# Kernel tuning notes

Hardware: AMD Instinct MI355X
Metric: run time of the kernel (lower is better)

Reference implementation:

```python
import jax, jax.numpy as jnp
import numpy as np

V = 100000   # vocab_size
E = 256      # embedding_dim
H = 256      # hidden_dim // 2 (per direction)
T = 32       # tagset_size
S = 4096     # seq_len
START, STOP = 30, 31
NEG = -10000.0


def setup_inputs() -> dict:
    key = jax.random.key(0)
    ks = jax.random.split(key, 13)
    sentence = jax.random.randint(ks[0], (S,), 0, V)
    h0 = jax.random.normal(ks[1], (2, H), dtype=jnp.float32)
    c0 = jax.random.normal(ks[2], (2, H), dtype=jnp.float32)
    embedding = jax.random.normal(ks[3], (V, E), dtype=jnp.float32) * 0.1
    # LSTM params, PyTorch layout: gates [i, f, g, o], combined bias = b_ih + b_hh
    w_ih_f = jax.random.normal(ks[4], (4 * H, E), dtype=jnp.float32) * 0.05
    w_hh_f = jax.random.normal(ks[5], (4 * H, H), dtype=jnp.float32) * 0.05
    b_f = jax.random.normal(ks[6], (4 * H,), dtype=jnp.float32) * 0.05
    w_ih_b = jax.random.normal(ks[7], (4 * H, E), dtype=jnp.float32) * 0.05
    w_hh_b = jax.random.normal(ks[8], (4 * H, H), dtype=jnp.float32) * 0.05
    b_b = jax.random.normal(ks[9], (4 * H,), dtype=jnp.float32) * 0.05
    lin_w = jax.random.normal(ks[10], (T, 2 * H), dtype=jnp.float32) * 0.05
    lin_b = jax.random.normal(ks[11], (T,), dtype=jnp.float32) * 0.05
    transitions = jax.random.normal(ks[12], (T, T), dtype=jnp.float32)
    transitions = transitions.at[START, :].set(NEG).at[:, STOP].set(NEG)
    return {"sentence": sentence, "h0": h0, "c0": c0, "embedding": embedding,
            "w_ih_f": w_ih_f, "w_hh_f": w_hh_f, "b_f": b_f,
            "w_ih_b": w_ih_b, "w_hh_b": w_hh_b, "b_b": b_b,
            "lin_w": lin_w, "lin_b": lin_b, "transitions": transitions}


def _lstm_dir(emb, h0, c0, w_ih, w_hh, b):
    # Precompute input contribution for all timesteps: [S, 4H]
    xg = emb @ w_ih.T + b

    def step(carry, xt):
        h, c = carry
        g = xt + h @ w_hh.T
        i, f, gg, o = jnp.split(g, 4)
        i = jax.nn.sigmoid(i); f = jax.nn.sigmoid(f)
        gg = jnp.tanh(gg); o = jax.nn.sigmoid(o)
        c = f * c + i * gg
        h = o * jnp.tanh(c)
        return (h, c), h

    _, hs = jax.lax.scan(step, (h0, c0), xg)
    return hs  # [S, H]


def reference(sentence, h0, c0, embedding, w_ih_f, w_hh_f, b_f,
              w_ih_b, w_hh_b, b_b, lin_w, lin_b, transitions):
    emb = embedding[sentence]                                    # [S, E]
    hs_f = _lstm_dir(emb, h0[0], c0[0], w_ih_f, w_hh_f, b_f)     # [S, H]
    hs_b = _lstm_dir(emb[::-1], h0[1], c0[1], w_ih_b, w_hh_b, b_b)[::-1]
    feats = jnp.concatenate([hs_f, hs_b], axis=-1) @ lin_w.T + lin_b  # [S, T]

    # Viterbi: forward_var over tags, vectorized over next/prev tags
    init = jnp.full((T,), NEG, dtype=feats.dtype).at[START].set(0.0)

    def vit_step(fv, feat):
        scores = fv[None, :] + transitions    # [next_tag, prev_tag]
        bp = jnp.argmax(scores, axis=1)       # best prev for each next tag
        fv_new = jnp.max(scores, axis=1) + feat
        return fv_new, bp

    fv, bps = jax.lax.scan(vit_step, init, feats)  # bps: [S, T]
    final = fv + transitions[STOP]
    last = jnp.argmax(final)
    score = final[last]

    # Backtrack (reverse scan); outputs[t] = best tag at timestep t
    def back_step(idx, bp):
        return bp[idx], idx

    _, path = jax.lax.scan(back_step, last, bps, reverse=True)
    return score, path
```

## Files before the change

### kernel.cpp

```cpp
#include <hip/hip_runtime.h>
#include <cstdint>
#include <cstddef>

#define S 4096
#define E 256
#define H 256
#define T 32
#define START_TAG 30
#define STOP_TAG 31
#define NEGV (-10000.0f)

typedef _Float16 half_t;
typedef _Float16 h2 __attribute__((ext_vector_type(2)));
typedef _Float16 f16x8 __attribute__((ext_vector_type(8)));
typedef float f32x4 __attribute__((ext_vector_type(4)));

__device__ __forceinline__ unsigned short f2h16(float f) {
    half_t h = (half_t)f;
    unsigned short u; __builtin_memcpy(&u, &h, 2); return u;
}
__device__ __forceinline__ float h16tof(unsigned short u) {
    half_t h; __builtin_memcpy(&h, &u, 2); return (float)h;
}

__device__ __forceinline__ float sigmoidf_(float x) {
    return 1.0f / (1.0f + __expf(-x));
}
__device__ __forceinline__ float tanhf_(float x) {
    return 1.0f - 2.0f / (__expf(2.0f * x) + 1.0f);
}

__device__ __forceinline__ f16x8 cvt8(float4 a, float4 b) {
    f16x8 v;
    v[0] = (_Float16)a.x; v[1] = (_Float16)a.y; v[2] = (_Float16)a.z; v[3] = (_Float16)a.w;
    v[4] = (_Float16)b.x; v[5] = (_Float16)b.y; v[6] = (_Float16)b.z; v[7] = (_Float16)b.w;
    return v;
}

#define SBLK 16
__global__ __launch_bounds__(256) void xg_kernel(
    const int* __restrict__ sent, const float* __restrict__ emb,
    const float* __restrict__ w_ih_f, const float* __restrict__ b_f,
    const float* __restrict__ w_ih_b, const float* __restrict__ b_b,
    unsigned short* __restrict__ xg16s)
{
    const int dir = blockIdx.y;
    const int t0 = blockIdx.x * SBLK;
    const float* w_ih = dir ? w_ih_b : w_ih_f;
    const float* bias = dir ? b_b : b_f;

    __shared__ float embs[SBLK][E];
    for (int p = threadIdx.x; p < SBLK * (E / 4); p += 256) {
        int r = p >> 6, kq = p & 63;
        int t = t0 + r;
        int tt = dir ? (S - 1 - t) : t;
        int tok = sent[tt];
        float4 v = *(const float4*)(emb + (size_t)tok * E + 4 * kq);
        *(float4*)&embs[r][4 * kq] = v;
    }
    __syncthreads();

    for (int jj = 0; jj < 4; ++jj) {
        int j = jj * 256 + threadIdx.x;
        const float* wrow = w_ih + (size_t)j * E;
        float bv = bias[j];
        float acc[SBLK];
        #pragma unroll
        for (int t = 0; t < SBLK; ++t) acc[t] = bv;

        for (int kc = 0; kc < E / 16; ++kc) {
            float w[16];
            float4 a0 = *(const float4*)(wrow + kc * 16);
            float4 a1 = *(const float4*)(wrow + kc * 16 + 4);
            float4 a2 = *(const float4*)(wrow + kc * 16 + 8);
            float4 a3 = *(const float4*)(wrow + kc * 16 + 12);
            float wv[16] = { a0.x, a0.y, a0.z, a0.w, a1.x, a1.y, a1.z, a1.w,
                             a2.x, a2.y, a2.z, a2.w, a3.x, a3.y, a3.z, a3.w };
            #pragma unroll
            for (int q = 0; q < 16; ++q) w[q] = wv[q];
            #pragma unroll
            for (int t = 0; t < SBLK; ++t) {
                const float* er = &embs[t][kc * 16];
                float s = 0.f;
                #pragma unroll
                for (int q = 0; q < 16; ++q) s += w[q] * er[q];
                acc[t] += s;
            }
        }
        const int u = threadIdx.x;
        #pragma unroll
        for (int t = 0; t < SBLK; ++t) {
            size_t base = (((size_t)dir * S + (size_t)(t0 + t)) * 256 + u) * 4 + jj;
            xg16s[base] = f2h16(acc[t]);
        }
    }
}

#define WLDS_BYTES (8 * 8 * 2 * 64 * 16)
#define LSTM_LDS_BYTES (WLDS_BYTES + 2 * 256 * 2)

__global__ __launch_bounds__(512, 2) void lstm_kernel(
    const float* __restrict__ h0, const float* __restrict__ c0,
    const float* __restrict__ w_hh_f, const float* __restrict__ w_hh_b,
    const unsigned long long* __restrict__ xgq, float* __restrict__ hs)
{
    extern __shared__ char smem[];

    const int dir  = blockIdx.x;
    const int tid  = threadIdx.x;
    const int lane = tid & 63;
    const int w    = tid >> 6;
    const int n    = lane & 15;
    const int kg   = lane >> 4;
    const float* w_hh = dir ? w_hh_b : w_hh_f;

    char* fragp = smem + ((size_t)w * 16 * 1024) + (size_t)lane * 16;

    f16x8 wR[8][6];
    #pragma unroll
    for (int c = 0; c < 8; ++c) {
        const int row = (c & 3) * 256 + w * 32 + 2 * n + (c >> 2);
        const float* pr = w_hh + (size_t)row * H + kg * 8;
        #pragma unroll
        for (int kt = 0; kt < 6; ++kt) {
            float4 a = *(const float4*)(pr + kt * 32);
            float4 b = *(const float4*)(pr + kt * 32 + 4);
            wR[c][kt] = cvt8(a, b);
        }
        #pragma unroll
        for (int j = 0; j < 2; ++j) {
            float4 a = *(const float4*)(pr + (6 + j) * 32);
            float4 b = *(const float4*)(pr + (6 + j) * 32 + 4);
            f16x8 v = cvt8(a, b);
            *(f16x8*)(fragp + (c * 2 + j) * 1024) = v;
        }
    }

    const int  u_a    = w * 32 + 2 * n;
    const bool hiU    = (kg >= 2);
    const int  u_own  = u_a + (hiU ? 1 : 0);
    const bool writer = (kg == 0) || (kg == 2);
    float cst = c0[dir * H + u_own];

    _Float16* hb0 = (_Float16*)(smem + WLDS_BYTES);
    if (tid < 256) hb0[tid] = (_Float16)h0[dir * H + tid];

    const unsigned long long* xgl = xgq + (size_t)dir * S * 256 + u_own;
    unsigned long long xgw = xgl[0];

    __syncthreads();

    for (int t = 0; t < S; ++t) {
        const char* hbp = smem + WLDS_BYTES + ((t & 1) << 9) + kg * 16;

        const int tn = (t + 1 < S) ? (t + 1) : t;
        unsigned long long xgn = xgl[(size_t)tn * 256];

        f32x4 acc[8];
        const f32x4 zc = { 0.f, 0.f, 0.f, 0.f };

        {
            f16x8 hA6 = *(const f16x8*)(hbp + 6 * 64);
            f16x8 hA7 = *(const f16x8*)(hbp + 7 * 64);
            #pragma unroll
            for (int c = 0; c < 8; ++c) {
                f16x8 w6 = *(const f16x8*)(fragp + (c * 2 + 0) * 1024);
                f16x8 w7 = *(const f16x8*)(fragp + (c * 2 + 1) * 1024);
                acc[c] = __builtin_amdgcn_mfma_f32_16x16x32_f16(hA6, w6, zc, 0, 0, 0);
                acc[c] = __builtin_amdgcn_mfma_f32_16x16x32_f16(hA7, w7, acc[c], 0, 0, 0);
            }
        }
        #pragma unroll
        for (int kt = 0; kt < 6; ++kt) {
            f16x8 hA = *(const f16x8*)(hbp + kt * 64);
            #pragma unroll
            for (int c = 0; c < 8; ++c)
                acc[c] = __builtin_amdgcn_mfma_f32_16x16x32_f16(hA, wR[c][kt], acc[c], 0, 0, 0);
        }

        unsigned int lo = (unsigned int)xgw;
        unsigned int hi = (unsigned int)(xgw >> 32);

        float gi = (hiU ? acc[4][0] : acc[0][0]) + h16tof((unsigned short)(lo & 0xffffu));
        float gf = (hiU ? acc[5][0] : acc[1][0]) + h16tof((unsigned short)(lo >> 16));
        float gg = (hiU ? acc[6][0] : acc[2][0]) + h16tof((unsigned short)(hi & 0xffffu));
        float go = (hiU ? acc[7][0] : acc[3][0]) + h16tof((unsigned short)(hi >> 16));

        float iv = sigmoidf_(gi);
        float fv = sigmoidf_(gf);
        float gv = tanhf_(gg);
        float ov = sigmoidf_(go);
        cst = fv * cst + iv * gv;
        float hv = ov * tanhf_(cst);

        if (writer) {
            *(_Float16*)(smem + WLDS_BYTES + (((t + 1) & 1) << 9) + u_own * 2) = (_Float16)hv;
            int row = dir ? (S - 1 - t) : t;
            hs[(size_t)row * 512 + dir * 256 + u_own] = hv;
        }
        xgw = xgn;
        __syncthreads();
    }
}

__global__ __launch_bounds__(256) void feats_kernel(
    const float* __restrict__ hs, const float* __restrict__ lin_w,
    const float* __restrict__ lin_b, float* __restrict__ feats)
{
    const int t0 = blockIdx.x * 8;
    __shared__ float rows[8][512];
    for (int p = threadIdx.x; p < 8 * 128; p += 256) {
        int r = p >> 7, sg = p & 127;
        float4 v = *(const float4*)(hs + (size_t)(t0 + r) * 512 + sg * 4);
        *(float4*)&rows[r][sg * 4] = v;
    }
    __syncthreads();

    const int tl = threadIdx.x >> 5, tag = threadIdx.x & 31;
    const float* lw = lin_w + (size_t)tag * 512;
    float acc = lin_b[tag];
    for (int kc = 0; kc < 32; ++kc) {
        float4 a0 = *(const float4*)(lw + kc * 16);
        float4 a1 = *(const float4*)(lw + kc * 16 + 4);
        float4 a2 = *(const float4*)(lw + kc * 16 + 8);
        float4 a3 = *(const float4*)(lw + kc * 16 + 12);
        const float* er = &rows[tl][kc * 16];
        acc += a0.x * er[0] + a0.y * er[1] + a0.z * er[2] + a0.w * er[3];
        acc += a1.x * er[4] + a1.y * er[5] + a1.z * er[6] + a1.w * er[7];
        acc += a2.x * er[8] + a2.y * er[9] + a2.z * er[10] + a2.w * er[11];
        acc += a3.x * er[12] + a3.y * er[13] + a3.z * er[14] + a3.w * er[15];
    }
    feats[(size_t)(t0 + tl) * T + tag] = acc;
}

#define VCS 64
#define VNC (S / VCS)
__global__ __launch_bounds__(256) void vit_chunk_kernel(
    const float* __restrict__ feats, const float* __restrict__ trans,
    float* __restrict__ gM)
{
    const int c = blockIdx.x;
    const int tid = threadIdx.x;
    const int n = tid >> 3, p0 = (tid & 7) * 4;
    __shared__ float Mb[2][32][36];

    float tr[32];
    #pragma unroll
    for (int k = 0; k < 32; ++k) tr[k] = trans[n * 32 + k];

    float f0 = feats[(size_t)(c * VCS) * 32 + n];
    float4 cur = { tr[p0] + f0, tr[p0 + 1] + f0, tr[p0 + 2] + f0, tr[p0 + 3] + f0 };
    *(float4*)&Mb[0][n][p0] = cur;
    __syncthreads();

    int rb = 0;
    for (int s = 1; s < VCS; ++s) {
        float fn = feats[(size_t)(c * VCS + s) * 32 + n];
        float4 acc = { -3.0e38f, -3.0e38f, -3.0e38f, -3.0e38f };
        #pragma unroll 8
        for (int k = 0; k < 32; ++k) {
            float4 mo = *(const float4*)&Mb[rb][k][p0];
            float tk = tr[k];
            acc.x = fmaxf(acc.x, tk + mo.x);
            acc.y = fmaxf(acc.y, tk + mo.y);
            acc.z = fmaxf(acc.z, tk + mo.z);
            acc.w = fmaxf(acc.w, tk + mo.w);
        }
        acc.x += fn; acc.y += fn; acc.z += fn; acc.w += fn;
        cur = acc;
        *(float4*)&Mb[rb ^ 1][n][p0] = acc;
        rb ^= 1;
        __syncthreads();
    }
    *(float4*)(gM + (size_t)c * 1024 + n * 32 + p0) = cur;
}

__global__ __launch_bounds__(1024) void vit_combine_kernel(
    const float* __restrict__ feats, const float* __restrict__ trans,
    const float* __restrict__ gM, unsigned char* __restrict__ gbp,
    float* __restrict__ out)
{
    __shared__ float MS[1024];
    __shared__ __align__(16) float bfv[VNC + 1][32];
    __shared__ __align__(16) float fvc[VNC][32];
    __shared__ unsigned char Mmap[VNC][32];
    __shared__ int ent[VNC];
    __shared__ int lastsh;

    const int tid = threadIdx.x;

    if (tid < 32) bfv[0][tid] = (tid == START_TAG) ? 0.f : NEGV;
    __syncthreads();
    for (int c = 0; c < VNC; ++c) {
        MS[tid] = gM[(size_t)c * 1024 + tid];
        __syncthreads();
        if (tid < 32) {
            float m = -3.0e38f;
            #pragma unroll 8
            for (int k = 0; k < 32; ++k)
                m = fmaxf(m, MS[tid * 32 + k] + bfv[c][k]);
            bfv[c + 1][tid] = m;
        }
        __syncthreads();
    }
    if (tid == 0) {
        float bm = -3.0e38f; int bl = 0;
        for (int j = 0; j < 32; ++j) {
            float s2 = bfv[VNC][j] + trans[STOP_TAG * 32 + j];
            if (s2 > bm) { bm = s2; bl = j; }
        }
        out[0] = bm;
        lastsh = bl;
    }
    __syncthreads();

    for (int pass = 0; pass < 2; ++pass) {
        const int c = (tid >> 5) + pass * 32;
        const int nt = tid & 31;
        float tr[32];
        #pragma unroll
        for (int k = 0; k < 32; ++k) tr[k] = trans[nt * 32 + k];

        fvc[c][nt] = bfv[c][nt];
        __builtin_amdgcn_wave_barrier();
        asm volatile("" ::: "memory");

        for (int s = 0; s < VCS; ++s) {
            const int t = c * VCS + s;
            float4 v0 = *(const float4*)&fvc[c][0];
            float4 v1 = *(const float4*)&fvc[c][4];
            float4 v2 = *(const float4*)&fvc[c][8];
            float4 v3 = *(const float4*)&fvc[c][12];
            float4 v4 = *(const float4*)&fvc[c][16];
            float4 v5 = *(const float4*)&fvc[c][20];
            float4 v6 = *(const float4*)&fvc[c][24];
            float4 v7 = *(const float4*)&fvc[c][28];
            float fvv[32] = { v0.x, v0.y, v0.z, v0.w, v1.x, v1.y, v1.z, v1.w,
                              v2.x, v2.y, v2.z, v2.w, v3.x, v3.y, v3.z, v3.w,
                              v4.x, v4.y, v4.z, v4.w, v5.x, v5.y, v5.z, v5.w,
                              v6.x, v6.y, v6.z, v6.w, v7.x, v7.y, v7.z, v7.w };
            float m = -3.0e38f; int bi = 0;
            #pragma unroll
            for (int k = 0; k < 32; ++k) {
                float s2 = fvv[k] + tr[k];
                if (s2 > m) { m = s2; bi = k; }
            }
            m += feats[(size_t)t * 32 + nt];
            gbp[(size_t)t * 32 + nt] = (unsigned char)bi;
            __builtin_amdgcn_wave_barrier();
            asm volatile("" ::: "memory");
            fvc[c][nt] = m;
            __builtin_amdgcn_wave_barrier();
            asm volatile("" ::: "memory");
        }
        __syncthreads();
    }

    {
        #pragma unroll
        for (int kk = 0; kk < 2; ++kk) {
            int it = tid + kk * 1024;
            int cc = it >> 5, st = it & 31;
            int cur = st;
            for (int s = VCS - 1; s >= 0; --s)
                cur = gbp[(size_t)(cc * VCS + s) * 32 + cur];
            Mmap[cc][st] = (unsigned char)cur;
        }
    }
    __syncthreads();

    if (tid == 0) {
        int cur = lastsh;
        ent[VNC - 1] = cur;
        for (int cchunk = VNC - 1; cchunk > 0; --cchunk) {
            cur = Mmap[cchunk][cur];
            ent[cchunk - 1] = cur;
        }
    }
    __syncthreads();

    if (tid < VNC) {
        int cur = ent[tid];
        for (int i = VCS - 1; i >= 0; --i) {
            int t = tid * VCS + i;
            out[1 + t] = (float)cur;
            cur = gbp[(size_t)t * 32 + cur];
        }
    }
}

extern "C" void kernel_launch(void* const* d_in, const int* in_sizes, int n_in,
                              void* d_out, int out_size, void* d_ws, size_t ws_size,
                              hipStream_t stream)
{
    const int* sent      = (const int*)d_in[0];
    const float* h0      = (const float*)d_in[1];
    const float* c0      = (const float*)d_in[2];
    const float* emb     = (const float*)d_in[3];
    const float* w_ih_f  = (const float*)d_in[4];
    const float* w_hh_f  = (const float*)d_in[5];
    const float* b_f     = (const float*)d_in[6];
    const float* w_ih_b  = (const float*)d_in[7];
    const float* w_hh_b  = (const float*)d_in[8];
    const float* b_b     = (const float*)d_in[9];
    const float* lin_w   = (const float*)d_in[10];
    const float* lin_b   = (const float*)d_in[11];
    const float* trans   = (const float*)d_in[12];
    float* out = (float*)d_out;

    unsigned long long* xgq = (unsigned long long*)d_ws;
    float* hs    = (float*)(xgq + (size_t)2 * S * 256);
    float* feats = hs + (size_t)S * 512;
    float* gM    = feats + (size_t)S * T;
    unsigned char* gbp = (unsigned char*)(gM + (size_t)VNC * 1024);

    hipFuncSetAttribute((const void*)lstm_kernel,
                        hipFuncAttributeMaxDynamicSharedMemorySize, LSTM_LDS_BYTES);

    xg_kernel<<<dim3(S / SBLK, 2), 256, 0, stream>>>(sent, emb, w_ih_f, b_f, w_ih_b, b_b,
                                                     (unsigned short*)xgq);
    lstm_kernel<<<2, 512, LSTM_LDS_BYTES, stream>>>(h0, c0, w_hh_f, w_hh_b, xgq, hs);
    feats_kernel<<<S / 8, 256, 0, stream>>>(hs, lin_w, lin_b, feats);
    vit_chunk_kernel<<<VNC, 256, 0, stream>>>(feats, trans, gM);
    vit_combine_kernel<<<1, 1024, 0, stream>>>(feats, trans, gM, gbp, out);
}
```

Baseline: 6.312 ms.

## Stream one k-tile of recurrent weights from global/L2 instead of LDS

Adds a prep kernel that packs the k-tile 6 fragments of w_hh into fp16 MFMA layout in global memory. The LSTM kernel now keeps only k-tile 7 in LDS and reloads the k-tile 6 fragments from global (cached in L2) every timestep, interleaving the loads with the MFMA chain. The aim is to cut per-step LDS traffic on the serial recurrence by moving part of the weight reads to the vector memory path. The cost is global-load latency inside the critical loop, plus one extra kernel launch.

```diff
diff --git a/kernel.cpp b/kernel.cpp
--- a/kernel.cpp
+++ b/kernel.cpp
@@ -11,7 +11,6 @@
 #define NEGV (-10000.0f)
 
 typedef _Float16 half_t;
-typedef _Float16 h2 __attribute__((ext_vector_type(2)));
 typedef _Float16 f16x8 __attribute__((ext_vector_type(8)));
 typedef float f32x4 __attribute__((ext_vector_type(4)));
 
@@ -35,6 +34,30 @@
     v[0] = (_Float16)a.x; v[1] = (_Float16)a.y; v[2] = (_Float16)a.z; v[3] = (_Float16)a.w;
     v[4] = (_Float16)b.x; v[5] = (_Float16)b.y; v[6] = (_Float16)b.z; v[7] = (_Float16)b.w;
     return v;
+}
+
+__global__ __launch_bounds__(512) void wprep_kernel(
+    const float* __restrict__ w_hh_f, const float* __restrict__ w_hh_b,
+    uint4* __restrict__ frag6)
+{
+    const int dir  = blockIdx.x;
+    const int tid  = threadIdx.x;
+    const int lane = tid & 63;
+    const int w    = tid >> 6;
+    const int n    = lane & 15;
+    const int kg   = lane >> 4;
+    const float* w_hh = dir ? w_hh_b : w_hh_f;
+
+    #pragma unroll
+    for (int c = 0; c < 8; ++c) {
+        const int row = (c & 3) * 256 + w * 32 + 2 * n + (c >> 2);
+        const float* pr = w_hh + (size_t)row * H + 6 * 32 + kg * 8;
+        float4 a = *(const float4*)(pr);
+        float4 b = *(const float4*)(pr + 4);
+        f16x8 v = cvt8(a, b);
+        uint4 u; __builtin_memcpy(&u, &v, 16);
+        frag6[((size_t)(dir * 8 + w) * 8 + c) * 64 + lane] = u;
+    }
 }
 
 #define SBLK 16
@@ -96,13 +119,14 @@
     }
 }
 
-#define WLDS_BYTES (8 * 8 * 2 * 64 * 16)
+#define WLDS_BYTES (8 * 8 * 64 * 16)
 #define LSTM_LDS_BYTES (WLDS_BYTES + 2 * 256 * 2)
 
 __global__ __launch_bounds__(512, 2) void lstm_kernel(
     const float* __restrict__ h0, const float* __restrict__ c0,
     const float* __restrict__ w_hh_f, const float* __restrict__ w_hh_b,
-    const unsigned long long* __restrict__ xgq, float* __restrict__ hs)
+    const unsigned long long* __restrict__ xgq, const uint4* __restrict__ frag6,
+    float* __restrict__ hs)
 {
     extern __shared__ char smem[];
 
@@ -114,7 +138,7 @@
     const int kg   = lane >> 4;
     const float* w_hh = dir ? w_hh_b : w_hh_f;
 
-    char* fragp = smem + ((size_t)w * 16 * 1024) + (size_t)lane * 16;
+    char* fragp = smem + ((size_t)w * 8192) + (size_t)lane * 16;
 
     f16x8 wR[8][6];
     #pragma unroll
@@ -127,12 +151,11 @@
             float4 b = *(const float4*)(pr + kt * 32 + 4);
             wR[c][kt] = cvt8(a, b);
         }
-        #pragma unroll
-        for (int j = 0; j < 2; ++j) {
-            float4 a = *(const float4*)(pr + (6 + j) * 32);
-            float4 b = *(const float4*)(pr + (6 + j) * 32 + 4);
+        {
+            float4 a = *(const float4*)(pr + 7 * 32);
+            float4 b = *(const float4*)(pr + 7 * 32 + 4);
             f16x8 v = cvt8(a, b);
-            *(f16x8*)(fragp + (c * 2 + j) * 1024) = v;
+            *(f16x8*)(fragp + c * 1024) = v;
         }
     }
 
@@ -148,11 +171,20 @@
     const unsigned long long* xgl = xgq + (size_t)dir * S * 256 + u_own;
     unsigned long long xgw = xgl[0];
 
+    const uint4* fgp = frag6 + (size_t)(dir * 8 + w) * 8 * 64 + lane;
+
     __syncthreads();
 
     for (int t = 0; t < S; ++t) {
         const char* hbp = smem + WLDS_BYTES + ((t & 1) << 9) + kg * 16;
 
+        const uint4* fg0 = fgp;
+        asm volatile("" : "+v"(fg0));
+        uint4 g0 = fg0[0 * 64];
+        uint4 g1 = fg0[1 * 64];
+        uint4 g2 = fg0[2 * 64];
+        uint4 g3 = fg0[3 * 64];
+
         const int tn = (t + 1 < S) ? (t + 1) : t;
         unsigned long long xgn = xgl[(size_t)tn * 256];
 
@@ -160,18 +192,52 @@
         const f32x4 zc = { 0.f, 0.f, 0.f, 0.f };
 
         {
-            f16x8 hA6 = *(const f16x8*)(hbp + 6 * 64);
             f16x8 hA7 = *(const f16x8*)(hbp + 7 * 64);
             #pragma unroll
             for (int c = 0; c < 8; ++c) {
-                f16x8 w6 = *(const f16x8*)(fragp + (c * 2 + 0) * 1024);
-                f16x8 w7 = *(const f16x8*)(fragp + (c * 2 + 1) * 1024);
-                acc[c] = __builtin_amdgcn_mfma_f32_16x16x32_f16(hA6, w6, zc, 0, 0, 0);
-                acc[c] = __builtin_amdgcn_mfma_f32_16x16x32_f16(hA7, w7, acc[c], 0, 0, 0);
+                f16x8 wx = *(const f16x8*)(fragp + c * 1024);
+                acc[c] = __builtin_amdgcn_mfma_f32_16x16x32_f16(hA7, wx, zc, 0, 0, 0);
             }
         }
-        #pragma unroll
-        for (int kt = 0; kt < 6; ++kt) {
+
+        f16x8 hA6 = *(const f16x8*)(hbp + 6 * 64);
+        {
+            f16x8 w0, w1, w2, w3;
+            __builtin_memcpy(&w0, &g0, 16); __builtin_memcpy(&w1, &g1, 16);
+            __builtin_memcpy(&w2, &g2, 16); __builtin_memcpy(&w3, &g3, 16);
+            acc[0] = __builtin_amdgcn_mfma_f32_16x16x32_f16(hA6, w0, acc[0], 0, 0, 0);
+            acc[1] = __builtin_amdgcn_mfma_f32_16x16x32_f16(hA6, w1, acc[1], 0, 0, 0);
+            acc[2] = __builtin_amdgcn_mfma_f32_16x16x32_f16(hA6, w2, acc[2], 0, 0, 0);
+            acc[3] = __builtin_amdgcn_mfma_f32_16x16x32_f16(hA6, w3, acc[3], 0, 0, 0);
+        }
+
+        const uint4* fg1 = fgp + 4 * 64;
+        asm volatile("" : "+v"(fg1));
+        g0 = fg1[0 * 64];
+        g1 = fg1[1 * 64];
+        g2 = fg1[2 * 64];
+        g3 = fg1[3 * 64];
+
+        #pragma unroll
+        for (int kt = 0; kt < 3; ++kt) {
+            f16x8 hA = *(const f16x8*)(hbp + kt * 64);
+            #pragma unroll
+            for (int c = 0; c < 8; ++c)
+                acc[c] = __builtin_amdgcn_mfma_f32_16x16x32_f16(hA, wR[c][kt], acc[c], 0, 0, 0);
+        }
+
+        {
+            f16x8 w4, w5, w6, w7;
+            __builtin_memcpy(&w4, &g0, 16); __builtin_memcpy(&w5, &g1, 16);
+            __builtin_memcpy(&w6, &g2, 16); __builtin_memcpy(&w7, &g3, 16);
+            acc[4] = __builtin_amdgcn_mfma_f32_16x16x32_f16(hA6, w4, acc[4], 0, 0, 0);
+            acc[5] = __builtin_amdgcn_mfma_f32_16x16x32_f16(hA6, w5, acc[5], 0, 0, 0);
+            acc[6] = __builtin_amdgcn_mfma_f32_16x16x32_f16(hA6, w6, acc[6], 0, 0, 0);
+            acc[7] = __builtin_amdgcn_mfma_f32_16x16x32_f16(hA6, w7, acc[7], 0, 0, 0);
+        }
+
+        #pragma unroll
+        for (int kt = 3; kt < 6; ++kt) {
             f16x8 hA = *(const f16x8*)(hbp + kt * 64);
             #pragma unroll
             for (int c = 0; c < 8; ++c)
@@ -413,13 +479,15 @@
     float* feats = hs + (size_t)S * 512;
     float* gM    = feats + (size_t)S * T;
     unsigned char* gbp = (unsigned char*)(gM + (size_t)VNC * 1024);
+    uint4* frag6 = (uint4*)(gbp + (size_t)S * 32);
 
     hipFuncSetAttribute((const void*)lstm_kernel,
                         hipFuncAttributeMaxDynamicSharedMemorySize, LSTM_LDS_BYTES);
 
+    wprep_kernel<<<2, 512, 0, stream>>>(w_hh_f, w_hh_b, frag6);
     xg_kernel<<<dim3(S / SBLK, 2), 256, 0, stream>>>(sent, emb, w_ih_f, b_f, w_ih_b, b_b,
                                                      (unsigned short*)xgq);
-    lstm_kernel<<<2, 512, LSTM_LDS_BYTES, stream>>>(h0, c0, w_hh_f, w_hh_b, xgq, hs);
+    lstm_kernel<<<2, 512, LSTM_LDS_BYTES, stream>>>(h0, c0, w_hh_f, w_hh_b, xgq, frag6, hs);
     feats_kernel<<<S / 8, 256, 0, stream>>>(hs, lin_w, lin_b, feats);
     vit_chunk_kernel<<<VNC, 256, 0, stream>>>(feats, trans, gM);
     vit_combine_kernel<<<1, 1024, 0, stream>>>(feats, trans, gM, gbp, out);
```

Result: slower. 7.622 ms (+20.8%).

## Split recurrent matvec K-range between MFMA and VALU dot2 paths

Applied to the files above, without the earlier changes.

The recurrent h@W_hh product previously ran entirely on MFMA over 8 K-tiles (6 held in registers, 2 read from LDS). Now MFMA covers only 6 K-tiles (4 in registers, 2 in LDS). The last 64 hidden inputs are computed per lane with packed fp16 dot2 instructions on weights held in registers, and the two halves are combined with a cross-lane shuffle. The aim is to shorten the serial MFMA chain on each timestep by running part of the reduction on the vector ALU in parallel. The cost is extra VALU work, more LDS reads and register pressure, and the writer lanes change from kg 0/2 to kg 0/1.

```diff
diff --git a/kernel.cpp b/kernel.cpp
--- a/kernel.cpp
+++ b/kernel.cpp
@@ -15,6 +15,12 @@
 typedef _Float16 f16x8 __attribute__((ext_vector_type(8)));
 typedef float f32x4 __attribute__((ext_vector_type(4)));
 
+__device__ __forceinline__ h2 f2h2(float a, float b) {
+    h2 r; r[0] = (half_t)a; r[1] = (half_t)b; return r;
+}
+__device__ __forceinline__ h2 u2h2(unsigned int u) {
+    h2 r; __builtin_memcpy(&r, &u, 4); return r;
+}
 __device__ __forceinline__ unsigned short f2h16(float f) {
     half_t h = (half_t)f;
     unsigned short u; __builtin_memcpy(&u, &h, 2); return u;
@@ -22,6 +28,16 @@
 __device__ __forceinline__ float h16tof(unsigned short u) {
     half_t h; __builtin_memcpy(&h, &u, 2); return (float)h;
 }
+
+#if __has_builtin(__builtin_amdgcn_fdot2)
+__device__ __forceinline__ float dot2(h2 a, h2 b, float c) {
+    return __builtin_amdgcn_fdot2(a, b, c, false);
+}
+#else
+__device__ __forceinline__ float dot2(h2 a, h2 b, float c) {
+    return c + (float)a[0] * (float)b[0] + (float)a[1] * (float)b[1];
+}
+#endif
 
 __device__ __forceinline__ float sigmoidf_(float x) {
     return 1.0f / (1.0f + __expf(-x));
@@ -116,31 +132,47 @@
 
     char* fragp = smem + ((size_t)w * 16 * 1024) + (size_t)lane * 16;
 
-    f16x8 wR[8][6];
+    f16x8 wR[8][4];
     #pragma unroll
     for (int c = 0; c < 8; ++c) {
         const int row = (c & 3) * 256 + w * 32 + 2 * n + (c >> 2);
         const float* pr = w_hh + (size_t)row * H + kg * 8;
         #pragma unroll
-        for (int kt = 0; kt < 6; ++kt) {
+        for (int kt = 0; kt < 4; ++kt) {
             float4 a = *(const float4*)(pr + kt * 32);
             float4 b = *(const float4*)(pr + kt * 32 + 4);
             wR[c][kt] = cvt8(a, b);
         }
         #pragma unroll
         for (int j = 0; j < 2; ++j) {
-            float4 a = *(const float4*)(pr + (6 + j) * 32);
-            float4 b = *(const float4*)(pr + (6 + j) * 32 + 4);
+            float4 a = *(const float4*)(pr + (4 + j) * 32);
+            float4 b = *(const float4*)(pr + (4 + j) * 32 + 4);
             f16x8 v = cvt8(a, b);
             *(f16x8*)(fragp + (c * 2 + j) * 1024) = v;
         }
     }
 
-    const int  u_a    = w * 32 + 2 * n;
-    const bool hiU    = (kg >= 2);
-    const int  u_own  = u_a + (hiU ? 1 : 0);
-    const bool writer = (kg == 0) || (kg == 2);
+    const int  par    = kg & 1;
+    const int  u_own  = w * 32 + 2 * n + par;
+    const bool writer = (kg < 2);
+    const int  ktvoff = 384 + ((kg >> 1) << 6);
     float cst = c0[dir * H + u_own];
+
+    h2 wV0[16], wV1[16], wV2[16], wV3[16];
+    {
+        const int ktv = 6 + (kg >> 1);
+        #pragma unroll
+        for (int g = 0; g < 4; ++g) {
+            const float* pr = w_hh + (size_t)(g * 256 + u_own) * H + ktv * 32;
+            h2* dst = (g == 0) ? wV0 : (g == 1) ? wV1 : (g == 2) ? wV2 : wV3;
+            #pragma unroll
+            for (int q = 0; q < 8; ++q) {
+                float4 a = *(const float4*)(pr + 4 * q);
+                dst[2 * q]     = f2h2(a.x, a.y);
+                dst[2 * q + 1] = f2h2(a.z, a.w);
+            }
+        }
+    }
 
     _Float16* hb0 = (_Float16*)(smem + WLDS_BYTES);
     if (tid < 256) hb0[tid] = (_Float16)h0[dir * H + tid];
@@ -151,7 +183,8 @@
     __syncthreads();
 
     for (int t = 0; t < S; ++t) {
-        const char* hbp = smem + WLDS_BYTES + ((t & 1) << 9) + kg * 16;
+        const char* hbase = smem + WLDS_BYTES + ((t & 1) << 9);
+        const char* hbp = hbase + kg * 16;
 
         const int tn = (t + 1 < S) ? (t + 1) : t;
         unsigned long long xgn = xgl[(size_t)tn * 256];
@@ -160,31 +193,67 @@
         const f32x4 zc = { 0.f, 0.f, 0.f, 0.f };
 
         {
-            f16x8 hA6 = *(const f16x8*)(hbp + 6 * 64);
-            f16x8 hA7 = *(const f16x8*)(hbp + 7 * 64);
+            f16x8 hA4 = *(const f16x8*)(hbp + 4 * 64);
+            f16x8 hA5 = *(const f16x8*)(hbp + 5 * 64);
             #pragma unroll
             for (int c = 0; c < 8; ++c) {
-                f16x8 w6 = *(const f16x8*)(fragp + (c * 2 + 0) * 1024);
-                f16x8 w7 = *(const f16x8*)(fragp + (c * 2 + 1) * 1024);
-                acc[c] = __builtin_amdgcn_mfma_f32_16x16x32_f16(hA6, w6, zc, 0, 0, 0);
-                acc[c] = __builtin_amdgcn_mfma_f32_16x16x32_f16(hA7, w7, acc[c], 0, 0, 0);
-            }
-        }
-        #pragma unroll
-        for (int kt = 0; kt < 6; ++kt) {
+                f16x8 w4 = *(const f16x8*)(fragp + (c * 2 + 0) * 1024);
+                f16x8 w5 = *(const f16x8*)(fragp + (c * 2 + 1) * 1024);
+                acc[c] = __builtin_amdgcn_mfma_f32_16x16x32_f16(hA4, w4, zc, 0, 0, 0);
+                acc[c] = __builtin_amdgcn_mfma_f32_16x16x32_f16(hA5, w5, acc[c], 0, 0, 0);
+            }
+        }
+        #pragma unroll
+        for (int kt = 0; kt < 4; ++kt) {
             f16x8 hA = *(const f16x8*)(hbp + kt * 64);
             #pragma unroll
             for (int c = 0; c < 8; ++c)
                 acc[c] = __builtin_amdgcn_mfma_f32_16x16x32_f16(hA, wR[c][kt], acc[c], 0, 0, 0);
         }
 
+        float mi = par ? acc[4][0] : acc[0][0];
+        float mf = par ? acc[5][0] : acc[1][0];
+        float mg = par ? acc[6][0] : acc[2][0];
+        float mo = par ? acc[7][0] : acc[3][0];
+
+        float p0 = 0.f, p1 = 0.f, p2 = 0.f, p3 = 0.f;
+        {
+            const char* hvb = hbase + ktvoff;
+            uint4 ha = *(const uint4*)(hvb);
+            uint4 hb = *(const uint4*)(hvb + 16);
+            h2 hh[8] = { u2h2(ha.x), u2h2(ha.y), u2h2(ha.z), u2h2(ha.w),
+                         u2h2(hb.x), u2h2(hb.y), u2h2(hb.z), u2h2(hb.w) };
+            #pragma unroll
+            for (int j = 0; j < 8; ++j) {
+                p0 = dot2(wV0[j], hh[j], p0);
+                p1 = dot2(wV1[j], hh[j], p1);
+                p2 = dot2(wV2[j], hh[j], p2);
+                p3 = dot2(wV3[j], hh[j], p3);
+            }
+            uint4 hc = *(const uint4*)(hvb + 32);
+            uint4 hd = *(const uint4*)(hvb + 48);
+            h2 hh2[8] = { u2h2(hc.x), u2h2(hc.y), u2h2(hc.z), u2h2(hc.w),
+                          u2h2(hd.x), u2h2(hd.y), u2h2(hd.z), u2h2(hd.w) };
+            #pragma unroll
+            for (int j = 0; j < 8; ++j) {
+                p0 = dot2(wV0[8 + j], hh2[j], p0);
+                p1 = dot2(wV1[8 + j], hh2[j], p1);
+                p2 = dot2(wV2[8 + j], hh2[j], p2);
+                p3 = dot2(wV3[8 + j], hh2[j], p3);
+            }
+            p0 += __shfl_xor(p0, 32);
+            p1 += __shfl_xor(p1, 32);
+            p2 += __shfl_xor(p2, 32);
+            p3 += __shfl_xor(p3, 32);
+        }
+
         unsigned int lo = (unsigned int)xgw;
         unsigned int hi = (unsigned int)(xgw >> 32);
 
-        float gi = (hiU ? acc[4][0] : acc[0][0]) + h16tof((unsigned short)(lo & 0xffffu));
-        float gf = (hiU ? acc[5][0] : acc[1][0]) + h16tof((unsigned short)(lo >> 16));
-        float gg = (hiU ? acc[6][0] : acc[2][0]) + h16tof((unsigned short)(hi & 0xffffu));
-        float go = (hiU ? acc[7][0] : acc[3][0]) + h16tof((unsigned short)(hi >> 16));
+        float gi = mi + p0 + h16tof((unsigned short)(lo & 0xffffu));
+        float gf = mf + p1 + h16tof((unsigned short)(lo >> 16));
+        float gg = mg + p2 + h16tof((unsigned short)(hi & 0xffffu));
+        float go = mo + p3 + h16tof((unsigned short)(hi >> 16));
 
         float iv = sigmoidf_(gi);
         float fv = sigmoidf_(gf);
```

Measured after the change: 7.265 ms. 15.1% more time.
